# Kernel optimization log

Measured on AMD Instinct MI355X. Metric: run time of the kernel, lower is better.

## Reference

```python
import jax, jax.numpy as jnp
import numpy as np


def _gcn_norm(edge_index, num_nodes, dtype):
    # PyG GCNConv.norm: add self-loops (weight 1), symmetric deg^{-1/2} normalization
    row, col = edge_index[0], edge_index[1]
    loop = jnp.arange(num_nodes, dtype=row.dtype)
    row = jnp.concatenate([row, loop])
    col = jnp.concatenate([col, loop])
    ew = jnp.ones(row.shape[0], dtype=dtype)
    deg = jax.ops.segment_sum(ew, row, num_segments=num_nodes)
    dis = jnp.where(deg > 0, jax.lax.rsqrt(deg), 0.0)
    norm = dis[row] * ew * dis[col]
    return row, col, norm


def _masked_gcn_conv(x, row, col, norm, sigma, W, b, num_nodes):
    # mask_features: edge gather -> diff/sigma -> square -> scatter-add -> exp mask
    h = (x[col] - x[row]) / sigma            # [E, F]
    h = norm[:, None] * h * h                # [E, F]
    mask = jax.ops.segment_sum(h, row, num_segments=num_nodes)        # [N, F]
    deg = jax.ops.segment_sum(jnp.ones_like(norm), row, num_segments=num_nodes)  # degree(source), >=1 due to self-loops
    x = x * jnp.exp(-mask / deg[:, None])
    # GCNConv: linear transform then normalized aggregation source->target
    xw = x @ W                               # [N, O]
    out = jax.ops.segment_sum(norm[:, None] * xw[row], col, num_segments=num_nodes)
    return out + b


def setup_inputs() -> dict:
    key = jax.random.key(0)
    ks = jax.random.split(key, 8)
    N, E, F, H, C = 100000, 1600000, 128, 64, 40
    g = 1.414  # xavier gain used for sigma
    return {
        "x": jax.random.normal(ks[0], (N, F), jnp.float32),
        "edge_index": jax.random.randint(ks[1], (2, E), 0, N, jnp.int64),
        "sigma1": jax.random.uniform(ks[2], (1, F), jnp.float32, -1.0, 1.0) * (g * np.sqrt(6.0 / (1 + F))),
        "W1": jax.random.normal(ks[3], (F, H), jnp.float32) * (1.0 / np.sqrt(F)),
        "b1": jnp.zeros((H,), jnp.float32),
        "sigma2": jax.random.uniform(ks[4], (1, H), jnp.float32, -1.0, 1.0) * (g * np.sqrt(6.0 / (1 + H))),
        "W2": jax.random.normal(ks[5], (H, C), jnp.float32) * (1.0 / np.sqrt(H)),
        "b2": jnp.zeros((C,), jnp.float32),
    }


def reference(x, edge_index, sigma1, W1, b1, sigma2, W2, b2):
    N = x.shape[0]
    row, col, norm = _gcn_norm(edge_index, N, x.dtype)
    x = _masked_gcn_conv(x, row, col, norm, sigma1, W1, b1, N)
    x = jax.nn.relu(x)
    # dropout is identity in eval mode
    x = _masked_gcn_conv(x, row, col, norm, sigma2, W2, b2, N)
    return jax.nn.log_softmax(x, axis=1)
```

## Files before the change

kernel.cpp:

```cpp
#include <hip/hip_runtime.h>
#include <cmath>

constexpr int F1 = 128;
constexpr int H  = 64;
constexpr int NC = 40;
constexpr int NXCD = 8;

constexpr int SCAN_TPB = 256;
constexpr int SCAN_IPT = 8;
constexpr int SCAN_EPB = SCAN_TPB * SCAN_IPT;

__global__ void isg_kernel(const float* __restrict__ s1, float* __restrict__ i1,
                           const float* __restrict__ s2, float* __restrict__ i2) {
    int i = threadIdx.x;
    if (i < F1) i1[i] = 1.0f / s1[i];
    if (i < H)  i2[i] = 1.0f / s2[i];
}

__global__ void count8_kernel(const int* __restrict__ row, const int* __restrict__ col,
                              int* __restrict__ cntO, int* __restrict__ cntI,
                              int E, int chunk, int stride) {
    int p = blockIdx.x & (NXCD - 1);
    int gid = blockIdx.x >> 3;
    unsigned lo = (unsigned)(p * chunk);
    for (int e = gid * blockDim.x + threadIdx.x; e < E; e += stride) {
        int r = row[e], c = col[e];
        if ((unsigned)r - lo < (unsigned)chunk) atomicAdd(&cntO[r], 1);
        if ((unsigned)c - lo < (unsigned)chunk) atomicAdd(&cntI[c], 1);
    }
}

__global__ void scan_partial_kernel(const int* __restrict__ cnt, int* __restrict__ bsum, int M) {
    __shared__ int red[SCAN_TPB];
    int t = threadIdx.x;
    int i0 = blockIdx.x * SCAN_EPB + t * SCAN_IPT;
    int s = 0;
#pragma unroll
    for (int k = 0; k < SCAN_IPT; ++k) {
        int i = i0 + k;
        if (i < M) s += cnt[i];
    }
    red[t] = s;
    __syncthreads();
    for (int off = SCAN_TPB / 2; off > 0; off >>= 1) {
        if (t < off) red[t] += red[t + off];
        __syncthreads();
    }
    if (t == 0) bsum[blockIdx.x] = red[0];
}

__global__ void scan_offsets_kernel(int* __restrict__ bsum, int nb,
                                    int* __restrict__ rowptrO, int* __restrict__ rowptrI,
                                    int N, int E) {
    __shared__ int sh[1024];
    int t = threadIdx.x;
    sh[t] = (t < nb) ? bsum[t] : 0;
    __syncthreads();
    for (int off = 1; off < 1024; off <<= 1) {
        int v = (t >= off) ? sh[t - off] : 0;
        __syncthreads();
        sh[t] += v;
        __syncthreads();
    }
    if (t < nb) bsum[t] = (t > 0) ? sh[t - 1] : 0;
    if (t == 0) { rowptrO[N] = E; rowptrI[N] = E; }
}

__global__ void scan_final_kernel(int* __restrict__ cntO, int* __restrict__ cntI,
                                  const int* __restrict__ bsum,
                                  int* __restrict__ rowptrO, int* __restrict__ rowptrI,
                                  float* __restrict__ dis, int N, int E) {
    __shared__ int sh[SCAN_TPB];
    int t = threadIdx.x;
    int M = 2 * N;
    const int* cnt = cntO;
    int i0 = blockIdx.x * SCAN_EPB + t * SCAN_IPT;
    int cv[SCAN_IPT], pre[SCAN_IPT];
    int run = 0;
#pragma unroll
    for (int k = 0; k < SCAN_IPT; ++k) {
        int i = i0 + k;
        cv[k] = (i < M) ? cnt[i] : 0;
        pre[k] = run;
        run += cv[k];
    }
    sh[t] = run;
    __syncthreads();
    for (int off = 1; off < SCAN_TPB; off <<= 1) {
        int v = (t >= off) ? sh[t - off] : 0;
        __syncthreads();
        sh[t] += v;
        __syncthreads();
    }
    int toff = ((t > 0) ? sh[t - 1] : 0) + bsum[blockIdx.x];
#pragma unroll
    for (int k = 0; k < SCAN_IPT; ++k) {
        int i = i0 + k;
        if (i < M) {
            int val = toff + pre[k];
            if (i < N) {
                rowptrO[i] = val;
                cntO[i] = val;
                dis[i] = rsqrtf((float)(cv[k] + 1));
            } else {
                rowptrI[i - N] = val - E;
                cntI[i - N] = val - E;
            }
        }
    }
}

__global__ void build8_kernel(const int* __restrict__ row, const int* __restrict__ col,
                              int* __restrict__ curO, int* __restrict__ curI,
                              int* __restrict__ adjO, int* __restrict__ adjI,
                              int E, int chunk, int stride) {
    int p = blockIdx.x & (NXCD - 1);
    int gid = blockIdx.x >> 3;
    unsigned lo = (unsigned)(p * chunk);
    for (int e = gid * blockDim.x + threadIdx.x; e < E; e += stride) {
        int r = row[e], c = col[e];
        if ((unsigned)r - lo < (unsigned)chunk) adjO[atomicAdd(&curO[r], 1)] = c;
        if ((unsigned)c - lo < (unsigned)chunk) adjI[atomicAdd(&curI[c], 1)] = r;
    }
}

template<int F, int O, int R>
__global__ void fused_mask_gemm_kernel(const int* __restrict__ rowptr, const int* __restrict__ adj,
                                       const float* __restrict__ dis, const float* __restrict__ x,
                                       const float* __restrict__ isg, const float* __restrict__ W,
                                       float* __restrict__ Y, int N) {
    constexpr int NT = R * 64;
    constexpr int G = F / 4;
    constexpr int NPI = 64 / G;
    __shared__ __align__(16) float Ws[F * O];
    __shared__ __align__(16) float Xs[R][F];
    int tid = threadIdx.x;
    for (int i = tid; i < F * O; i += NT) Ws[i] = W[i];

    int w = tid >> 6, lane = tid & 63;
    int h = lane / G;
    int j = lane % G;
    int r = blockIdx.x * R + w;
    if (r < N) {
        int beg = rowptr[r], end = rowptr[r + 1];
        float dr = dis[r];
        float inv_deg = 1.0f / (float)(end - beg + 1);
        float4 xr = *(const float4*)&x[(size_t)r * F + 4 * j];
        float4 sg = *(const float4*)&isg[4 * j];
        float4 acc = {0.f, 0.f, 0.f, 0.f};
        for (int base = beg; base < end; base += 64) {
            int nn = min(64, end - base);
            int cl = 0; float dl = 0.0f;
            if (base + lane < end) { cl = adj[base + lane]; dl = dis[cl]; }
            for (int t = 0; t < nn; t += NPI) {
                int i = t + h;
                bool valid = i < nn;
                int ii = valid ? i : 0;
                int c = __shfl(cl, ii);
                float nrm = valid ? dr * __shfl(dl, ii) : 0.0f;
                float4 xc = *(const float4*)&x[(size_t)c * F + 4 * j];
                float d0 = (xc.x - xr.x) * sg.x;
                float d1 = (xc.y - xr.y) * sg.y;
                float d2 = (xc.z - xr.z) * sg.z;
                float d3 = (xc.w - xr.w) * sg.w;
                acc.x = fmaf(nrm * d0, d0, acc.x);
                acc.y = fmaf(nrm * d1, d1, acc.y);
                acc.z = fmaf(nrm * d2, d2, acc.z);
                acc.w = fmaf(nrm * d3, d3, acc.w);
            }
        }
#pragma unroll
        for (int off = G; off < 64; off <<= 1) {
            acc.x += __shfl_xor(acc.x, off);
            acc.y += __shfl_xor(acc.y, off);
            acc.z += __shfl_xor(acc.z, off);
            acc.w += __shfl_xor(acc.w, off);
        }
        if (h == 0) {
            float4 xm;
            xm.x = xr.x * expf(-acc.x * inv_deg);
            xm.y = xr.y * expf(-acc.y * inv_deg);
            xm.z = xr.z * expf(-acc.z * inv_deg);
            xm.w = xr.w * expf(-acc.w * inv_deg);
            *(float4*)&Xs[w][4 * j] = xm;
        }
    } else {
        if (h == 0) *(float4*)&Xs[w][4 * j] = {0.f, 0.f, 0.f, 0.f};
    }
    __syncthreads();

    int row0 = blockIdx.x * R;
    for (int idx = tid; idx < R * O; idx += NT) {
        int rr = idx / O, o = idx % O;
        if (row0 + rr < N) {
            float acc = 0.0f;
#pragma unroll
            for (int f = 0; f < F; ++f) acc = fmaf(Xs[rr][f], Ws[f * O + o], acc);
            Y[(size_t)(row0 + rr) * O + o] = acc;
        }
    }
}

template<int O, int MODE>
__global__ void agg_gather_kernel(const int* __restrict__ rowptr, const int* __restrict__ adj,
                                  const float* __restrict__ dis, const float* __restrict__ xw,
                                  const float* __restrict__ bias, float* __restrict__ out, int N) {
    int c = blockIdx.x * (blockDim.x >> 6) + (threadIdx.x >> 6);
    if (c >= N) return;
    int lane = threadIdx.x & 63;
    int j = lane & 31, h = lane >> 5;
    bool active = (2 * j < O);
    int beg = rowptr[c], end = rowptr[c + 1];
    float dc = dis[c];
    float ax = 0.f, ay = 0.f;
    if (h == 0 && active) {
        float2 v = *(const float2*)&xw[(size_t)c * O + 2 * j];
        ax = dc * dc * v.x; ay = dc * dc * v.y;
    }
    for (int base = beg; base < end; base += 64) {
        int nn = min(64, end - base);
        int rl = 0; float dl = 0.0f;
        if (base + lane < end) { rl = adj[base + lane]; dl = dis[rl]; }
        for (int t = 0; t < nn; t += 2) {
            int i = t + h;
            bool valid = i < nn;
            int ii = valid ? i : 0;
            int rr = __shfl(rl, ii);
            float nrm = valid ? dc * __shfl(dl, ii) : 0.0f;
            if (active) {
                float2 v = *(const float2*)&xw[(size_t)rr * O + 2 * j];
                ax = fmaf(nrm, v.x, ax);
                ay = fmaf(nrm, v.y, ay);
            }
        }
    }
    ax += __shfl_xor(ax, 32);
    ay += __shfl_xor(ay, 32);
    if (MODE == 0) {
        if (h == 0 && active) {
            float2 bb = *(const float2*)&bias[2 * j];
            float2 o2;
            o2.x = fmaxf(ax + bb.x, 0.0f);
            o2.y = fmaxf(ay + bb.y, 0.0f);
            *(float2*)&out[(size_t)c * O + 2 * j] = o2;
        }
    } else {
        float vx = -INFINITY, vy = -INFINITY;
        if (active) {
            float2 bb = *(const float2*)&bias[2 * j];
            vx = ax + bb.x; vy = ay + bb.y;
        }
        float m = fmaxf(vx, vy);
#pragma unroll
        for (int off = 16; off > 0; off >>= 1) m = fmaxf(m, __shfl_xor(m, off));
        float s = active ? (expf(vx - m) + expf(vy - m)) : 0.0f;
#pragma unroll
        for (int off = 16; off > 0; off >>= 1) s += __shfl_xor(s, off);
        float ls = logf(s);
        if (h == 0 && active) {
            float2 o2 = {vx - m - ls, vy - m - ls};
            *(float2*)&out[(size_t)c * O + 2 * j] = o2;
        }
    }
}

extern "C" void kernel_launch(void* const* d_in, const int* in_sizes, int n_in,
                              void* d_out, int out_size, void* d_ws, size_t ws_size,
                              hipStream_t stream) {
    const float* x    = (const float*)d_in[0];
    const int*   ei   = (const int*)  d_in[1];
    const float* sig1 = (const float*)d_in[2];
    const float* W1   = (const float*)d_in[3];
    const float* b1   = (const float*)d_in[4];
    const float* sig2 = (const float*)d_in[5];
    const float* W2   = (const float*)d_in[6];
    const float* b2   = (const float*)d_in[7];
    float* out = (float*)d_out;

    const int N = in_sizes[0] / F1;
    const int E = in_sizes[1] / 2;
    const int* row = ei;
    const int* col = ei + E;

    char* w = (char*)d_ws;
    auto alloc = [&](size_t bytes) { void* q = w; w += (bytes + 255) & ~255ull; return q; };
    int*   cntO    = (int*)  alloc((size_t)2 * N * 4);
    int*   cntI    = cntO + N;
    int*   rowptrO = (int*)  alloc((size_t)(N + 1) * 4);
    int*   rowptrI = (int*)  alloc((size_t)(N + 1) * 4);
    int*   adjO    = (int*)  alloc((size_t)E * 4);
    int*   adjI    = (int*)  alloc((size_t)E * 4);
    float* dis     = (float*)alloc((size_t)N * 4);
    float* isg1    = (float*)alloc(F1 * 4);
    float* isg2    = (float*)alloc(H * 4);
    int*   bsum    = (int*)  alloc(1024 * 4);
    float* bufXW   = (float*)alloc((size_t)N * H * 4);
    float* bufH    = (float*)alloc((size_t)N * H * 4);
    float* bufXW2  = (float*)alloc((size_t)N * NC * 4);

    const int B = 256;
    const int chunk = (N + NXCD - 1) / NXCD;
    const int WPP = 1024;
    const int stride8 = WPP * B;
    dim3 g8(NXCD * WPP);
    const int M = 2 * N;
    const int nb = (M + SCAN_EPB - 1) / SCAN_EPB;

    hipMemsetAsync(cntO, 0, (size_t)2 * N * 4, stream);
    isg_kernel<<<1, 128, 0, stream>>>(sig1, isg1, sig2, isg2);
    count8_kernel<<<g8, B, 0, stream>>>(row, col, cntO, cntI, E, chunk, stride8);
    scan_partial_kernel<<<nb, SCAN_TPB, 0, stream>>>(cntO, bsum, M);
    scan_offsets_kernel<<<1, 1024, 0, stream>>>(bsum, nb, rowptrO, rowptrI, N, E);
    scan_final_kernel<<<nb, SCAN_TPB, 0, stream>>>(cntO, cntI, bsum, rowptrO, rowptrI, dis, N, E);
    build8_kernel<<<g8, B, 0, stream>>>(row, col, cntO, cntI, adjO, adjI, E, chunk, stride8);

    fused_mask_gemm_kernel<F1, H, 8><<<(N + 7) / 8, 512, 0, stream>>>(rowptrO, adjO, dis, x, isg1, W1, bufXW, N);
    agg_gather_kernel<H, 0><<<(N + 3) / 4, B, 0, stream>>>(rowptrI, adjI, dis, bufXW, b1, bufH, N);

    fused_mask_gemm_kernel<H, NC, 8><<<(N + 7) / 8, 512, 0, stream>>>(rowptrO, adjO, dis, bufH, isg2, W2, bufXW2, N);
    agg_gather_kernel<NC, 1><<<(N + 3) / 4, B, 0, stream>>>(rowptrI, adjI, dis, bufXW2, b2, out, N);
}
```

Before: 718.6 us.

## Gather pre-scaled bf16 features in mask kernels and widen aggregation vectors

Adds a prep kernel that stores x/sigma as bf16, and the first aggregation kernel now also emits a bf16 copy of its layer-1 output scaled by 1/sigma2. The mask kernels gather these half-size rows (8 features per lane) in place of fp32 x, which is meant to halve the random-gather traffic that dominates the edge loop. The aggregation kernels also switch from float2 to float4 loads with 4 edges in flight per wave. The cost is bf16 rounding in the mask exponent, one extra pass over x, and reuse of the u1 buffer as bufXW2.

```diff
diff --git a/kernel.cpp b/kernel.cpp
--- a/kernel.cpp
+++ b/kernel.cpp
@@ -9,12 +9,42 @@
 constexpr int SCAN_TPB = 256;
 constexpr int SCAN_IPT = 8;
 constexpr int SCAN_EPB = SCAN_TPB * SCAN_IPT;
+
+__device__ inline unsigned short f2bf(float f) {
+    union { float f; unsigned u; } v; v.f = f;
+    unsigned r = (v.u + 0x7FFFu + ((v.u >> 16) & 1u)) >> 16;
+    return (unsigned short)r;
+}
+__device__ inline float bflo(unsigned p) {
+    union { float f; unsigned u; } v; v.u = p << 16; return v.f;
+}
+__device__ inline float bfhi(unsigned p) {
+    union { float f; unsigned u; } v; v.u = p & 0xFFFF0000u; return v.f;
+}
 
 __global__ void isg_kernel(const float* __restrict__ s1, float* __restrict__ i1,
                            const float* __restrict__ s2, float* __restrict__ i2) {
     int i = threadIdx.x;
     if (i < F1) i1[i] = 1.0f / s1[i];
     if (i < H)  i2[i] = 1.0f / s2[i];
+}
+
+__global__ void prep_u_kernel(const float* __restrict__ x, const float* __restrict__ isg,
+                              unsigned short* __restrict__ u, size_t n8, int F) {
+    size_t idx = (size_t)blockIdx.x * blockDim.x + threadIdx.x;
+    if (idx >= n8) return;
+    size_t base = idx * 8;
+    int fk = (int)(base % (size_t)F);
+    float4 a0 = *(const float4*)&x[base];
+    float4 a1 = *(const float4*)&x[base + 4];
+    float4 s0 = *(const float4*)&isg[fk];
+    float4 s1 = *(const float4*)&isg[fk + 4];
+    uint4 p;
+    p.x = (unsigned)f2bf(a0.x * s0.x) | ((unsigned)f2bf(a0.y * s0.y) << 16);
+    p.y = (unsigned)f2bf(a0.z * s0.z) | ((unsigned)f2bf(a0.w * s0.w) << 16);
+    p.z = (unsigned)f2bf(a1.x * s1.x) | ((unsigned)f2bf(a1.y * s1.y) << 16);
+    p.w = (unsigned)f2bf(a1.z * s1.z) | ((unsigned)f2bf(a1.w * s1.w) << 16);
+    *(uint4*)&u[base] = p;
 }
 
 __global__ void count8_kernel(const int* __restrict__ row, const int* __restrict__ col,
@@ -127,10 +157,11 @@
 template<int F, int O, int R>
 __global__ void fused_mask_gemm_kernel(const int* __restrict__ rowptr, const int* __restrict__ adj,
                                        const float* __restrict__ dis, const float* __restrict__ x,
-                                       const float* __restrict__ isg, const float* __restrict__ W,
+                                       const unsigned short* __restrict__ u,
+                                       const float* __restrict__ W,
                                        float* __restrict__ Y, int N) {
     constexpr int NT = R * 64;
-    constexpr int G = F / 4;
+    constexpr int G = F / 8;
     constexpr int NPI = 64 / G;
     __shared__ __align__(16) float Ws[F * O];
     __shared__ __align__(16) float Xs[R][F];
@@ -145,9 +176,20 @@
         int beg = rowptr[r], end = rowptr[r + 1];
         float dr = dis[r];
         float inv_deg = 1.0f / (float)(end - beg + 1);
-        float4 xr = *(const float4*)&x[(size_t)r * F + 4 * j];
-        float4 sg = *(const float4*)&isg[4 * j];
-        float4 acc = {0.f, 0.f, 0.f, 0.f};
+        float xr[8], ur[8], acc[8];
+        {
+            float4 a0 = *(const float4*)&x[(size_t)r * F + 8 * j];
+            float4 a1 = *(const float4*)&x[(size_t)r * F + 8 * j + 4];
+            xr[0] = a0.x; xr[1] = a0.y; xr[2] = a0.z; xr[3] = a0.w;
+            xr[4] = a1.x; xr[5] = a1.y; xr[6] = a1.z; xr[7] = a1.w;
+            uint4 rr = *(const uint4*)&u[(size_t)r * F + 8 * j];
+            ur[0] = bflo(rr.x); ur[1] = bfhi(rr.x);
+            ur[2] = bflo(rr.y); ur[3] = bfhi(rr.y);
+            ur[4] = bflo(rr.z); ur[5] = bfhi(rr.z);
+            ur[6] = bflo(rr.w); ur[7] = bfhi(rr.w);
+        }
+#pragma unroll
+        for (int k = 0; k < 8; ++k) acc[k] = 0.0f;
         for (int base = beg; base < end; base += 64) {
             int nn = min(64, end - base);
             int cl = 0; float dl = 0.0f;
@@ -158,34 +200,36 @@
                 int ii = valid ? i : 0;
                 int c = __shfl(cl, ii);
                 float nrm = valid ? dr * __shfl(dl, ii) : 0.0f;
-                float4 xc = *(const float4*)&x[(size_t)c * F + 4 * j];
-                float d0 = (xc.x - xr.x) * sg.x;
-                float d1 = (xc.y - xr.y) * sg.y;
-                float d2 = (xc.z - xr.z) * sg.z;
-                float d3 = (xc.w - xr.w) * sg.w;
-                acc.x = fmaf(nrm * d0, d0, acc.x);
-                acc.y = fmaf(nrm * d1, d1, acc.y);
-                acc.z = fmaf(nrm * d2, d2, acc.z);
-                acc.w = fmaf(nrm * d3, d3, acc.w);
+                uint4 raw = *(const uint4*)&u[(size_t)c * F + 8 * j];
+                float uc[8];
+                uc[0] = bflo(raw.x); uc[1] = bfhi(raw.x);
+                uc[2] = bflo(raw.y); uc[3] = bfhi(raw.y);
+                uc[4] = bflo(raw.z); uc[5] = bfhi(raw.z);
+                uc[6] = bflo(raw.w); uc[7] = bfhi(raw.w);
+#pragma unroll
+                for (int k = 0; k < 8; ++k) {
+                    float d = uc[k] - ur[k];
+                    acc[k] = fmaf(nrm * d, d, acc[k]);
+                }
             }
         }
 #pragma unroll
         for (int off = G; off < 64; off <<= 1) {
-            acc.x += __shfl_xor(acc.x, off);
-            acc.y += __shfl_xor(acc.y, off);
-            acc.z += __shfl_xor(acc.z, off);
-            acc.w += __shfl_xor(acc.w, off);
+#pragma unroll
+            for (int k = 0; k < 8; ++k) acc[k] += __shfl_xor(acc[k], off);
         }
         if (h == 0) {
-            float4 xm;
-            xm.x = xr.x * expf(-acc.x * inv_deg);
-            xm.y = xr.y * expf(-acc.y * inv_deg);
-            xm.z = xr.z * expf(-acc.z * inv_deg);
-            xm.w = xr.w * expf(-acc.w * inv_deg);
-            *(float4*)&Xs[w][4 * j] = xm;
+            float xm[8];
+#pragma unroll
+            for (int k = 0; k < 8; ++k) xm[k] = xr[k] * expf(-acc[k] * inv_deg);
+            *(float4*)&Xs[w][8 * j]     = make_float4(xm[0], xm[1], xm[2], xm[3]);
+            *(float4*)&Xs[w][8 * j + 4] = make_float4(xm[4], xm[5], xm[6], xm[7]);
         }
     } else {
-        if (h == 0) *(float4*)&Xs[w][4 * j] = {0.f, 0.f, 0.f, 0.f};
+        if (h == 0) {
+            *(float4*)&Xs[w][8 * j]     = make_float4(0.f, 0.f, 0.f, 0.f);
+            *(float4*)&Xs[w][8 * j + 4] = make_float4(0.f, 0.f, 0.f, 0.f);
+        }
     }
     __syncthreads();
 
@@ -204,62 +248,76 @@
 template<int O, int MODE>
 __global__ void agg_gather_kernel(const int* __restrict__ rowptr, const int* __restrict__ adj,
                                   const float* __restrict__ dis, const float* __restrict__ xw,
-                                  const float* __restrict__ bias, float* __restrict__ out, int N) {
+                                  const float* __restrict__ bias, float* __restrict__ out,
+                                  unsigned short* __restrict__ u2, const float* __restrict__ isg2,
+                                  int N) {
     int c = blockIdx.x * (blockDim.x >> 6) + (threadIdx.x >> 6);
     if (c >= N) return;
     int lane = threadIdx.x & 63;
-    int j = lane & 31, h = lane >> 5;
-    bool active = (2 * j < O);
+    int j = lane & 15, h = lane >> 4;
+    bool active = (4 * j < O);
     int beg = rowptr[c], end = rowptr[c + 1];
     float dc = dis[c];
-    float ax = 0.f, ay = 0.f;
+    float4 a = {0.f, 0.f, 0.f, 0.f};
     if (h == 0 && active) {
-        float2 v = *(const float2*)&xw[(size_t)c * O + 2 * j];
-        ax = dc * dc * v.x; ay = dc * dc * v.y;
+        float4 v = *(const float4*)&xw[(size_t)c * O + 4 * j];
+        a.x = dc * dc * v.x; a.y = dc * dc * v.y;
+        a.z = dc * dc * v.z; a.w = dc * dc * v.w;
     }
     for (int base = beg; base < end; base += 64) {
         int nn = min(64, end - base);
         int rl = 0; float dl = 0.0f;
         if (base + lane < end) { rl = adj[base + lane]; dl = dis[rl]; }
-        for (int t = 0; t < nn; t += 2) {
+        for (int t = 0; t < nn; t += 4) {
             int i = t + h;
             bool valid = i < nn;
             int ii = valid ? i : 0;
             int rr = __shfl(rl, ii);
             float nrm = valid ? dc * __shfl(dl, ii) : 0.0f;
             if (active) {
-                float2 v = *(const float2*)&xw[(size_t)rr * O + 2 * j];
-                ax = fmaf(nrm, v.x, ax);
-                ay = fmaf(nrm, v.y, ay);
+                float4 v = *(const float4*)&xw[(size_t)rr * O + 4 * j];
+                a.x = fmaf(nrm, v.x, a.x);
+                a.y = fmaf(nrm, v.y, a.y);
+                a.z = fmaf(nrm, v.z, a.z);
+                a.w = fmaf(nrm, v.w, a.w);
             }
         }
     }
-    ax += __shfl_xor(ax, 32);
-    ay += __shfl_xor(ay, 32);
+    a.x += __shfl_xor(a.x, 16); a.x += __shfl_xor(a.x, 32);
+    a.y += __shfl_xor(a.y, 16); a.y += __shfl_xor(a.y, 32);
+    a.z += __shfl_xor(a.z, 16); a.z += __shfl_xor(a.z, 32);
+    a.w += __shfl_xor(a.w, 16); a.w += __shfl_xor(a.w, 32);
     if (MODE == 0) {
         if (h == 0 && active) {
-            float2 bb = *(const float2*)&bias[2 * j];
-            float2 o2;
-            o2.x = fmaxf(ax + bb.x, 0.0f);
-            o2.y = fmaxf(ay + bb.y, 0.0f);
-            *(float2*)&out[(size_t)c * O + 2 * j] = o2;
+            float4 bb = *(const float4*)&bias[4 * j];
+            float4 o4;
+            o4.x = fmaxf(a.x + bb.x, 0.0f);
+            o4.y = fmaxf(a.y + bb.y, 0.0f);
+            o4.z = fmaxf(a.z + bb.z, 0.0f);
+            o4.w = fmaxf(a.w + bb.w, 0.0f);
+            *(float4*)&out[(size_t)c * O + 4 * j] = o4;
+            float4 s4 = *(const float4*)&isg2[4 * j];
+            uint2 p;
+            p.x = (unsigned)f2bf(o4.x * s4.x) | ((unsigned)f2bf(o4.y * s4.y) << 16);
+            p.y = (unsigned)f2bf(o4.z * s4.z) | ((unsigned)f2bf(o4.w * s4.w) << 16);
+            *(uint2*)&u2[(size_t)c * O + 4 * j] = p;
         }
     } else {
-        float vx = -INFINITY, vy = -INFINITY;
+        float4 v = {-INFINITY, -INFINITY, -INFINITY, -INFINITY};
         if (active) {
-            float2 bb = *(const float2*)&bias[2 * j];
-            vx = ax + bb.x; vy = ay + bb.y;
-        }
-        float m = fmaxf(vx, vy);
-#pragma unroll
-        for (int off = 16; off > 0; off >>= 1) m = fmaxf(m, __shfl_xor(m, off));
-        float s = active ? (expf(vx - m) + expf(vy - m)) : 0.0f;
-#pragma unroll
-        for (int off = 16; off > 0; off >>= 1) s += __shfl_xor(s, off);
-        float ls = logf(s);
+            float4 bb = *(const float4*)&bias[4 * j];
+            v.x = a.x + bb.x; v.y = a.y + bb.y; v.z = a.z + bb.z; v.w = a.w + bb.w;
+        }
+        float m = fmaxf(fmaxf(v.x, v.y), fmaxf(v.z, v.w));
+#pragma unroll
+        for (int off = 8; off > 0; off >>= 1) m = fmaxf(m, __shfl_xor(m, off));
+        float s = active ? (expf(v.x - m) + expf(v.y - m) + expf(v.z - m) + expf(v.w - m)) : 0.0f;
+#pragma unroll
+        for (int off = 8; off > 0; off >>= 1) s += __shfl_xor(s, off);
+        float mls = m + logf(s);
         if (h == 0 && active) {
-            float2 o2 = {vx - m - ls, vy - m - ls};
-            *(float2*)&out[(size_t)c * O + 2 * j] = o2;
+            float4 o4 = {v.x - mls, v.y - mls, v.z - mls, v.w - mls};
+            *(float4*)&out[(size_t)c * O + 4 * j] = o4;
         }
     }
 }
@@ -294,9 +352,11 @@
     float* isg1    = (float*)alloc(F1 * 4);
     float* isg2    = (float*)alloc(H * 4);
     int*   bsum    = (int*)  alloc(1024 * 4);
+    unsigned short* u1 = (unsigned short*)alloc((size_t)N * F1 * 2);
+    unsigned short* u2 = (unsigned short*)alloc((size_t)N * H * 2);
     float* bufXW   = (float*)alloc((size_t)N * H * 4);
     float* bufH    = (float*)alloc((size_t)N * H * 4);
-    float* bufXW2  = (float*)alloc((size_t)N * NC * 4);
+    float* bufXW2  = (float*)u1;
 
     const int B = 256;
     const int chunk = (N + NXCD - 1) / NXCD;
@@ -308,15 +368,16 @@
 
     hipMemsetAsync(cntO, 0, (size_t)2 * N * 4, stream);
     isg_kernel<<<1, 128, 0, stream>>>(sig1, isg1, sig2, isg2);
+    prep_u_kernel<<<(int)(((size_t)N * F1 / 8 + B - 1) / B), B, 0, stream>>>(x, isg1, u1, (size_t)N * F1 / 8, F1);
     count8_kernel<<<g8, B, 0, stream>>>(row, col, cntO, cntI, E, chunk, stride8);
     scan_partial_kernel<<<nb, SCAN_TPB, 0, stream>>>(cntO, bsum, M);
     scan_offsets_kernel<<<1, 1024, 0, stream>>>(bsum, nb, rowptrO, rowptrI, N, E);
     scan_final_kernel<<<nb, SCAN_TPB, 0, stream>>>(cntO, cntI, bsum, rowptrO, rowptrI, dis, N, E);
     build8_kernel<<<g8, B, 0, stream>>>(row, col, cntO, cntI, adjO, adjI, E, chunk, stride8);
 
-    fused_mask_gemm_kernel<F1, H, 8><<<(N + 7) / 8, 512, 0, stream>>>(rowptrO, adjO, dis, x, isg1, W1, bufXW, N);
-    agg_gather_kernel<H, 0><<<(N + 3) / 4, B, 0, stream>>>(rowptrI, adjI, dis, bufXW, b1, bufH, N);
-
-    fused_mask_gemm_kernel<H, NC, 8><<<(N + 7) / 8, 512, 0, stream>>>(rowptrO, adjO, dis, bufH, isg2, W2, bufXW2, N);
-    agg_gather_kernel<NC, 1><<<(N + 3) / 4, B, 0, stream>>>(rowptrI, adjI, dis, bufXW2, b2, out, N);
-}
+    fused_mask_gemm_kernel<F1, H, 8><<<(N + 7) / 8, 512, 0, stream>>>(rowptrO, adjO, dis, x, u1, W1, bufXW, N);
+    agg_gather_kernel<H, 0><<<(N + 3) / 4, B, 0, stream>>>(rowptrI, adjI, dis, bufXW, b1, bufH, u2, isg2, N);
+
+    fused_mask_gemm_kernel<H, NC, 8><<<(N + 7) / 8, 512, 0, stream>>>(rowptrO, adjO, dis, bufH, u2, W2, bufXW2, N);
+    agg_gather_kernel<NC, 1><<<(N + 3) / 4, B, 0, stream>>>(rowptrI, adjI, dis, bufXW2, b2, out, nullptr, nullptr, N);
+}
```

Result: faster. 672.5 us (-6.4%).
